# Performance work log

Measured on AMD Instinct MI355X. Metric: run time of the kernel, lower is better.

The kernel has to match this reference:

```python
import jax
import jax.numpy as jnp
import numpy as np

N_WIRES = 4          # hardcoded by QLayer encoder (rx on wires 0..3)
H = N_WIRES          # hidden_dim must equal n_qubits for the gating elementwise math
T, B, D, TAGS = 512, 2048, 8, 16  # original unbinds dim 0, so dim0 = time, dim1 = batch


def apply_rx(state, theta, wire):
    """Apply RX(theta) on `wire`. state: (B,2,2,2,2) complex64, theta: (B,)."""
    st = jnp.moveaxis(state, 1 + wire, -1)
    a, b = st[..., 0], st[..., 1]
    th = theta[:, None, None, None] * 0.5
    c = jnp.cos(th)
    s = -1j * jnp.sin(th)
    st = jnp.stack([c * a + s * b, s * a + c * b], axis=-1)
    return jnp.moveaxis(st, -1, 1 + wire)


def apply_cnot(state, ctrl, tgt):
    st = jnp.moveaxis(state, (1 + ctrl, 1 + tgt), (-2, -1))  # (...,2,2)
    st = st.at[..., 1, :].set(st[..., 1, ::-1])
    return jnp.moveaxis(st, (-2, -1), (1 + ctrl, 1 + tgt))


def qlayer(angles, thetas):
    """QuantumQLSTM.QLayer: RX data encoding, trainable RX, CNOT ring, PauliZ expvals.
    angles: (B, 4) data angles; thetas: (4,) trainable RX angles -> (B, 4) expvals."""
    bsz = angles.shape[0]
    state = jnp.zeros((bsz, 16), jnp.complex64).at[:, 0].set(1.0)
    state = state.reshape(bsz, 2, 2, 2, 2)
    for w in range(N_WIRES):
        state = apply_rx(state, angles[:, w], w)
    for w in range(N_WIRES):
        state = apply_rx(state, jnp.broadcast_to(thetas[w], (bsz,)), w)
    for w in range(N_WIRES):  # cnot(w, w+1), last wraps to 0
        state = apply_cnot(state, w, (w + 1) % N_WIRES)
    probs = state.real ** 2 + state.imag ** 2  # (B,2,2,2,2)
    exps = []
    for w in range(N_WIRES):
        sign = jnp.array([1.0, -1.0], jnp.float32).reshape(
            [1] + [2 if i == w else 1 for i in range(N_WIRES)])
        exps.append(jnp.sum(probs * sign, axis=(1, 2, 3, 4)))
    return jnp.stack(exps, axis=-1)  # (B, 4)


def lstm_forward(x, w_gates, b_gates, rx_theta):
    # Faithful to torch: inputs.unbind(dim=0) -> scan over axis 0; batch = x.shape[1].
    bsz = x.shape[1]
    h0 = jnp.zeros((bsz, H), x.dtype)
    c0 = jnp.zeros((bsz, H), x.dtype)

    def step(carry, xt):
        hx, cx = carry
        comb = jnp.concatenate([xt, hx], axis=-1)                    # (B, D+H)
        pre = jnp.einsum('bd,gkd->gbk', comb, w_gates) + b_gates[:, None, :]  # (4,B,4)
        f = jax.nn.sigmoid(qlayer(pre[0], rx_theta[0]))
        i = jax.nn.sigmoid(qlayer(pre[1], rx_theta[1]))
        g = jnp.tanh(qlayer(pre[2], rx_theta[2]))
        o = jax.nn.sigmoid(qlayer(pre[3], rx_theta[3]))
        cx = f * cx + i * g
        hx = o * jnp.tanh(cx)
        return (hx, cx), hx

    _, outs = jax.lax.scan(jax.checkpoint(step), (h0, c0), x)
    return outs  # (T, B, H)


def setup_inputs() -> dict:
    key = jax.random.key(0)
    ks = jax.random.split(key, 6)
    x = jax.random.normal(ks[0], (T, B, D), jnp.float32)
    w_gates = jax.random.normal(ks[1], (4, N_WIRES, D + H), jnp.float32) * 0.3
    b_gates = jnp.zeros((4, N_WIRES), jnp.float32)
    rx_theta = jax.random.uniform(ks[2], (4, N_WIRES), jnp.float32, 0.0, 2.0 * np.pi)
    w_tag = jax.random.normal(ks[3], (TAGS, H), jnp.float32) * 0.3
    b_tag = jnp.zeros((TAGS,), jnp.float32)
    return {"x": x, "w_gates": w_gates, "b_gates": b_gates,
            "rx_theta": rx_theta, "w_tag": w_tag, "b_tag": b_tag}


def reference(x, w_gates, b_gates, rx_theta, w_tag, b_tag):
    # encode(): SamplerQNN has input_params=[], so it cannot transform features;
    # features pass through to the QLSTM (see notes).
    outs = lstm_forward(x, w_gates, b_gates, rx_theta)   # (T, B, H)
    logits = outs @ w_tag.T + b_tag                      # (T, B, TAGS)
    return jax.nn.log_softmax(logits, axis=-1)
```

## Files before the change

kernel.cpp:

```cpp
#include <hip/hip_runtime.h>

#define TT   512
#define BB   2048
#define NTAG 16
#define CH   8
#define NCH  (TT / CH)
#define BBN  (BB * NTAG)

typedef float v2f __attribute__((ext_vector_type(2)));

#define DPP_XOR1  0xB1
#define DPP_XOR2  0x4E
#define DPP_XOR3  0x1B
#define DPP_ROR4  0x124
#define DPP_ROR8  0x128
#define DPP_ROR12 0x12C

template<int CTRL>
__device__ __forceinline__ float dppf(float v) {
    int r = __builtin_amdgcn_update_dpp(0, __builtin_bit_cast(int, v),
                                        CTRL, 0xF, 0xF, true);
    return __builtin_bit_cast(float, r);
}

#define PINV(x) asm volatile("" : "+v"(x))

__global__ __launch_bounds__(256, 1) void qlstm_fused(
    const float* __restrict__ x,
    const float* __restrict__ w_gates,
    const float* __restrict__ b_gates,
    const float* __restrict__ rx_theta,
    const float* __restrict__ w_tag,
    const float* __restrict__ b_tag,
    float* __restrict__ out)
{
    __shared__ float  accL[2][2][CH][64];
    __shared__ float  hrng[2][2][CH][64];
    __shared__ float4 xstg[2][2][64];

    const int tid = threadIdx.x;
    const int wv  = tid >> 6;
    const int l   = tid & 63;
    const int e   = l >> 4;
    const int g   = (l >> 2) & 3;
    const int k   = l & 3;

    const float IV  = 0.15915494309189535f;
    const float L2E = 1.44269504088896f;
    const float LN2 = 0.69314718056f;

    if (wv < 2) {
        const int s = wv;

        const float* wrow = w_gates + (g * 4 + k) * 12;
        float wh0 = wrow[8 + (k ^ 0)] * IV;
        float wh1 = wrow[8 + (k ^ 1)] * IV;
        float wh2 = wrow[8 + (k ^ 2)] * IV;
        float wh3 = wrow[8 + (k ^ 3)] * IV;

        const bool gt = (g == 2);
        float ab = gt ? 0.0f : 0.5f;
        float d0 = gt ? 0.999904f  : 0.25f;
        float d1 = gt ? -0.331065f : -0.0208333333f;
        float d2 = gt ? 0.120472f  : 0.00208333333f;
        float d3 = gt ? -0.027717f : -2.10813e-4f;

        float u0 = 0.999160f,  u1 = -0.325289f, u2 = 0.112257f;
        float u3 = -0.028766f, u4 = 0.0043665f, u5 = -0.00028186f;

        const bool k0 = (k == 0), k1 = (k == 1), k3 = (k == 3);
        const bool g0 = (g == 0), g2 = (g == 2), glo = (g < 2);

        PINV(wh0); PINV(wh1); PINV(wh2); PINV(wh3);
        PINV(ab);  PINV(d0);  PINV(d1);  PINV(d2);  PINV(d3);
        PINV(u0);  PINV(u1);  PINV(u2);  PINV(u3);  PINV(u4);  PINV(u5);

        float h = 0.f, h1 = 0.f, h2 = 0.f, h3 = 0.f, c = 0.f;

        __syncthreads();

        for (int cc = 0; cc < NCH; ++cc) {
            const int cur = cc & 1;

            const float* ap = &accL[s][cur][0][l];
            float a0 = ap[0 * 64], a1 = ap[1 * 64];
            float a2 = ap[2 * 64], a3 = ap[3 * 64];
            float a4 = ap[4 * 64], a5 = ap[5 * 64];
            float a6 = ap[6 * 64], a7 = ap[7 * 64];
            asm volatile("" : "+v"(a0), "+v"(a1), "+v"(a2), "+v"(a3),
                             "+v"(a4), "+v"(a5), "+v"(a6), "+v"(a7));
            float a[CH] = { a0, a1, a2, a3, a4, a5, a6, a7 };

            float* hp = &hrng[s][cur][0][l];

            #pragma unroll
            for (int i = 0; i < CH; ++i) {
                float ang = fmaf(h,  wh0, a[i]);
                ang = fmaf(h1, wh1, ang);
                ang = fmaf(h2, wh2, ang);
                ang = fmaf(h3, wh3, ang);

                const float C = __builtin_amdgcn_cosf(ang);
                const float m1 = dppf<DPP_XOR1>(C);
                const float m2 = dppf<DPP_XOR2>(C);
                const float m3 = dppf<DPP_XOR3>(C);
                const float Bp  = m2 * m3;
                const float pp  = C * m1;
                const float F1  = k0 ? m1 : C;
                const float F1b = k3 ? pp : F1;
                const float F2  = k1 ? m1 : Bp;
                const float q   = F1b * F2;

                const float y  = q * q;
                const float y2 = y * y;
                const float tA = fmaf(y, d1, d0);
                const float tB = fmaf(y, d3, d2);
                const float P  = fmaf(y2, tB, tA);
                const float act = fmaf(q, P, ab);

                const float rA = dppf<DPP_ROR12>(act);
                const float rB = dppf<DPP_ROR8>(act);
                const float rC = dppf<DPP_ROR4>(act);
                const float f_ = glo ? (g0 ? act : rC) : (g2 ? rB : rA);
                const float i_ = glo ? (g0 ? rA : act) : (g2 ? rC : rB);
                const float gg = glo ? (g0 ? rB : rA) : (g2 ? act : rC);
                const float o_ = glo ? (g0 ? rC : rB) : (g2 ? rA : act);

                c = fmaf(f_, c, i_ * gg);

                const float cy  = c * c;
                const float cy2 = cy * cy;
                const float t1  = fmaf(cy, u1, u0);
                const float t2  = fmaf(cy, u3, u2);
                const float t3  = fmaf(cy, u5, u4);
                const float t4  = fmaf(cy2, t3, t2);
                const float Pc  = fmaf(cy2, t4, t1);
                const float voc = o_ * c;
                const float hr  = Pc * voc;

                hp[i * 64] = hr;

                h  = hr;
                h1 = dppf<DPP_XOR1>(hr);
                h2 = dppf<DPP_XOR2>(hr);
                h3 = dppf<DPP_XOR3>(hr);
            }
            __syncthreads();
        }
    } else {
        const int s  = wv - 2;
        const int b0 = blockIdx.x * 8 + s * 4;

        const float* wrow = w_gates + (g * 4 + k) * 12;
        const v2f wp0 = { wrow[0] * IV, wrow[1] * IV };
        const v2f wp1 = { wrow[2] * IV, wrow[3] * IV };
        const v2f wp2 = { wrow[4] * IV, wrow[5] * IV };
        const v2f wp3 = { wrow[6] * IV, wrow[7] * IV };
        const v2f bp  = { (b_gates[g * 4 + k] + rx_theta[g * 4 + k]) * IV, 0.0f };

        const int tag = g * 4 + k;
        const float wt0 = w_tag[tag * 4 + (k ^ 0)] * L2E;
        const float wt1 = w_tag[tag * 4 + (k ^ 1)] * L2E;
        const float wt2 = w_tag[tag * 4 + (k ^ 2)] * L2E;
        const float wt3 = w_tag[tag * 4 + (k ^ 3)] * L2E;
        const float bt  = b_tag[tag] * L2E;

        const int hsl = e * 16 + k;
        float* outp = out + (size_t)b0 * NTAG + l;

        const float* xlane = x + (size_t)(l >> 3) * (BB * 8)
                               + (size_t)b0 * 8 + (l & 7) * 4;
        const size_t CHOFF = (size_t)CH * BB * 8;

        float4 reg = *(const float4*)(xlane);
        xstg[s][0][l] = reg;
        reg = *(const float4*)(xlane + CHOFF);
        xstg[s][1][l] = reg;
        {
            float* ap = &accL[s][0][0][l];
            #pragma unroll
            for (int i = 0; i < CH; ++i) {
                const float4 xA = xstg[s][0][i * 8 + 2 * e];
                const float4 xB = xstg[s][0][i * 8 + 2 * e + 1];
                const v2f a01 = { xA.x, xA.y }, a23 = { xA.z, xA.w };
                const v2f a45 = { xB.x, xB.y }, a67 = { xB.z, xB.w };
                v2f acc = __builtin_elementwise_fma(a01, wp0, bp);
                acc = __builtin_elementwise_fma(a23, wp1, acc);
                acc = __builtin_elementwise_fma(a45, wp2, acc);
                acc = __builtin_elementwise_fma(a67, wp3, acc);
                ap[i * 64] = acc.x + acc.y;
            }
        }
        reg = *(const float4*)(xlane + 2 * CHOFF);
        __syncthreads();

        for (int cc = 0; cc < NCH; ++cc) {
            const int cur = cc & 1;

            if (cc + 2 < NCH) {
                xstg[s][cur][l] = reg;
                const int cn = (cc + 3 < NCH) ? cc + 3 : NCH - 1;
                reg = *(const float4*)(xlane + (size_t)cn * CHOFF);
            }

            if (cc + 1 < NCH) {
                float* ap = &accL[s][cur ^ 1][0][l];
                #pragma unroll
                for (int i = 0; i < CH; ++i) {
                    const float4 xA = xstg[s][cur ^ 1][i * 8 + 2 * e];
                    const float4 xB = xstg[s][cur ^ 1][i * 8 + 2 * e + 1];
                    const v2f a01 = { xA.x, xA.y }, a23 = { xA.z, xA.w };
                    const v2f a45 = { xB.x, xB.y }, a67 = { xB.z, xB.w };
                    v2f acc = __builtin_elementwise_fma(a01, wp0, bp);
                    acc = __builtin_elementwise_fma(a23, wp1, acc);
                    acc = __builtin_elementwise_fma(a45, wp2, acc);
                    acc = __builtin_elementwise_fma(a67, wp3, acc);
                    ap[i * 64] = acc.x + acc.y;
                }
            }

            if (cc > 0) {
                const float* hp = &hrng[s][cur ^ 1][0][hsl];
                #pragma unroll
                for (int i = 0; i < CH; ++i) {
                    const float hv = hp[i * 64];
                    const float q1 = dppf<DPP_XOR1>(hv);
                    const float q2 = dppf<DPP_XOR2>(hv);
                    const float q3 = dppf<DPP_XOR3>(hv);

                    const float lgq = fmaf(hv, wt0, fmaf(q1, wt1, fmaf(q2, wt2,
                                         fmaf(q3, wt3, bt))));
                    const float ex = __builtin_amdgcn_exp2f(lgq);
                    float sm = ex + dppf<DPP_XOR1>(ex);
                    sm = sm + dppf<DPP_XOR2>(sm);
                    sm = sm + dppf<DPP_ROR4>(sm);
                    sm = sm + dppf<DPP_ROR8>(sm);
                    const float l2s = __builtin_amdgcn_logf(sm);

                    *outp = (lgq - l2s) * LN2;
                    outp += BBN;
                }
            }
            __syncthreads();
        }

        {
            const float* hp = &hrng[s][1][0][hsl];
            #pragma unroll
            for (int i = 0; i < CH; ++i) {
                const float hv = hp[i * 64];
                const float q1 = dppf<DPP_XOR1>(hv);
                const float q2 = dppf<DPP_XOR2>(hv);
                const float q3 = dppf<DPP_XOR3>(hv);

                const float lgq = fmaf(hv, wt0, fmaf(q1, wt1, fmaf(q2, wt2,
                                     fmaf(q3, wt3, bt))));
                const float ex = __builtin_amdgcn_exp2f(lgq);
                float sm = ex + dppf<DPP_XOR1>(ex);
                sm = sm + dppf<DPP_XOR2>(sm);
                sm = sm + dppf<DPP_ROR4>(sm);
                sm = sm + dppf<DPP_ROR8>(sm);
                const float l2s = __builtin_amdgcn_logf(sm);

                *outp = (lgq - l2s) * LN2;
                outp += BBN;
            }
        }
    }
}

extern "C" void kernel_launch(void* const* d_in, const int* in_sizes, int n_in,
                              void* d_out, int out_size, void* d_ws, size_t ws_size,
                              hipStream_t stream) {
    const float* x        = (const float*)d_in[0];
    const float* w_gates  = (const float*)d_in[1];
    const float* b_gates  = (const float*)d_in[2];
    const float* rx_theta = (const float*)d_in[3];
    const float* w_tag    = (const float*)d_in[4];
    const float* b_tag    = (const float*)d_in[5];
    float* out = (float*)d_out;

    qlstm_fused<<<BB / 8, 256, 0, stream>>>(x, w_gates, b_gates, rx_theta,
                                            w_tag, b_tag, out);
}
```

Measured before the change: 146.4 us.

## Transpose recurrent lane mapping so gate gather uses DPP quad broadcasts

Changes the lane layout of the recurrent waves so each quad holds the four gates of one wire instead of the four wires of one gate. The gate combination then uses quad-broadcast DPP moves with no select chains, and the wire mixing uses row rotations. The angle sum is split into two partial chains to shorten the serial dependency. The accumulator read index and the h-slot index of the producer waves are remapped to match, which risks mismatched indexing.

```diff
diff --git a/kernel.cpp b/kernel.cpp
--- a/kernel.cpp
+++ b/kernel.cpp
@@ -15,6 +15,10 @@
 #define DPP_ROR4  0x124
 #define DPP_ROR8  0x128
 #define DPP_ROR12 0x12C
+#define DPP_BC0   0x00
+#define DPP_BC1   0x55
+#define DPP_BC2   0xAA
+#define DPP_BC3   0xFF
 
 template<int CTRL>
 __device__ __forceinline__ float dppf(float v) {
@@ -42,8 +46,6 @@
     const int wv  = tid >> 6;
     const int l   = tid & 63;
     const int e   = l >> 4;
-    const int g   = (l >> 2) & 3;
-    const int k   = l & 3;
 
     const float IV  = 0.15915494309189535f;
     const float L2E = 1.44269504088896f;
@@ -51,14 +53,16 @@
 
     if (wv < 2) {
         const int s = wv;
-
-        const float* wrow = w_gates + (g * 4 + k) * 12;
-        float wh0 = wrow[8 + (k ^ 0)] * IV;
-        float wh1 = wrow[8 + (k ^ 1)] * IV;
-        float wh2 = wrow[8 + (k ^ 2)] * IV;
-        float wh3 = wrow[8 + (k ^ 3)] * IV;
-
-        const bool gt = (g == 2);
+        const int w = (l >> 2) & 3;
+        const int G = l & 3;
+
+        const float* wrow = w_gates + (G * 4 + w) * 12;
+        float wh0 = wrow[8 + ((w + 0) & 3)] * IV;
+        float wh1 = wrow[8 + ((w + 1) & 3)] * IV;
+        float wh2 = wrow[8 + ((w + 2) & 3)] * IV;
+        float wh3 = wrow[8 + ((w + 3) & 3)] * IV;
+
+        const bool gt = (G == 2);
         float ab = gt ? 0.0f : 0.5f;
         float d0 = gt ? 0.999904f  : 0.25f;
         float d1 = gt ? -0.331065f : -0.0208333333f;
@@ -68,21 +72,22 @@
         float u0 = 0.999160f,  u1 = -0.325289f, u2 = 0.112257f;
         float u3 = -0.028766f, u4 = 0.0043665f, u5 = -0.00028186f;
 
-        const bool k0 = (k == 0), k1 = (k == 1), k3 = (k == 3);
-        const bool g0 = (g == 0), g2 = (g == 2), glo = (g < 2);
+        const bool w0 = (w == 0), w1 = (w == 1), w3 = (w == 3);
 
         PINV(wh0); PINV(wh1); PINV(wh2); PINV(wh3);
         PINV(ab);  PINV(d0);  PINV(d1);  PINV(d2);  PINV(d3);
         PINV(u0);  PINV(u1);  PINV(u2);  PINV(u3);  PINV(u4);  PINV(u5);
 
-        float h = 0.f, h1 = 0.f, h2 = 0.f, h3 = 0.f, c = 0.f;
+        const int atl = (l & 48) | ((l & 3) << 2) | ((l >> 2) & 3);
+
+        float h = 0.f, hg1 = 0.f, hg2 = 0.f, hg3 = 0.f, c = 0.f;
 
         __syncthreads();
 
         for (int cc = 0; cc < NCH; ++cc) {
             const int cur = cc & 1;
 
-            const float* ap = &accL[s][cur][0][l];
+            const float* ap = &accL[s][cur][0][atl];
             float a0 = ap[0 * 64], a1 = ap[1 * 64];
             float a2 = ap[2 * 64], a3 = ap[3 * 64];
             float a4 = ap[4 * 64], a5 = ap[5 * 64];
@@ -95,20 +100,22 @@
 
             #pragma unroll
             for (int i = 0; i < CH; ++i) {
-                float ang = fmaf(h,  wh0, a[i]);
-                ang = fmaf(h1, wh1, ang);
-                ang = fmaf(h2, wh2, ang);
-                ang = fmaf(h3, wh3, ang);
+                const float sA  = fmaf(h, wh0, a[i]);
+                const float td1 = fmaf(hg1, wh1, sA);
+                const float td2 = hg2 * wh2;
+                const float td3 = fmaf(hg3, wh3, td2);
+                const float ang = td1 + td3;
 
                 const float C = __builtin_amdgcn_cosf(ang);
-                const float m1 = dppf<DPP_XOR1>(C);
-                const float m2 = dppf<DPP_XOR2>(C);
-                const float m3 = dppf<DPP_XOR3>(C);
-                const float Bp  = m2 * m3;
-                const float pp  = C * m1;
-                const float F1  = k0 ? m1 : C;
-                const float F1b = k3 ? pp : F1;
-                const float F2  = k1 ? m1 : Bp;
+
+                const float n1 = dppf<DPP_ROR12>(C);
+                const float n2 = dppf<DPP_ROR8>(C);
+                const float n3 = dppf<DPP_ROR4>(C);
+                const float Bp = n2 * n3;
+                const float pp = C * n1;
+                const float F1  = w0 ? n1 : C;
+                const float F1b = w3 ? pp : F1;
+                const float F2  = w1 ? n3 : Bp;
                 const float q   = F1b * F2;
 
                 const float y  = q * q;
@@ -118,15 +125,12 @@
                 const float P  = fmaf(y2, tB, tA);
                 const float act = fmaf(q, P, ab);
 
-                const float rA = dppf<DPP_ROR12>(act);
-                const float rB = dppf<DPP_ROR8>(act);
-                const float rC = dppf<DPP_ROR4>(act);
-                const float f_ = glo ? (g0 ? act : rC) : (g2 ? rB : rA);
-                const float i_ = glo ? (g0 ? rA : act) : (g2 ? rC : rB);
-                const float gg = glo ? (g0 ? rB : rA) : (g2 ? act : rC);
-                const float o_ = glo ? (g0 ? rC : rB) : (g2 ? rA : act);
-
-                c = fmaf(f_, c, i_ * gg);
+                const float F_ = dppf<DPP_BC0>(act);
+                const float A1 = dppf<DPP_BC1>(act);
+                const float A2 = dppf<DPP_BC2>(act);
+                const float O_ = dppf<DPP_BC3>(act);
+
+                c = fmaf(F_, c, A1 * A2);
 
                 const float cy  = c * c;
                 const float cy2 = cy * cy;
@@ -135,21 +139,23 @@
                 const float t3  = fmaf(cy, u5, u4);
                 const float t4  = fmaf(cy2, t3, t2);
                 const float Pc  = fmaf(cy2, t4, t1);
-                const float voc = o_ * c;
+                const float voc = O_ * c;
                 const float hr  = Pc * voc;
 
                 hp[i * 64] = hr;
 
-                h  = hr;
-                h1 = dppf<DPP_XOR1>(hr);
-                h2 = dppf<DPP_XOR2>(hr);
-                h3 = dppf<DPP_XOR3>(hr);
+                h   = hr;
+                hg1 = dppf<DPP_ROR12>(hr);
+                hg2 = dppf<DPP_ROR8>(hr);
+                hg3 = dppf<DPP_ROR4>(hr);
             }
             __syncthreads();
         }
     } else {
         const int s  = wv - 2;
         const int b0 = blockIdx.x * 8 + s * 4;
+        const int g  = (l >> 2) & 3;
+        const int k  = l & 3;
 
         const float* wrow = w_gates + (g * 4 + k) * 12;
         const v2f wp0 = { wrow[0] * IV, wrow[1] * IV };
@@ -165,7 +171,7 @@
         const float wt3 = w_tag[tag * 4 + (k ^ 3)] * L2E;
         const float bt  = b_tag[tag] * L2E;
 
-        const int hsl = e * 16 + k;
+        const int hsl = e * 16 + k * 4;
         float* outp = out + (size_t)b0 * NTAG + l;
 
         const float* xlane = x + (size_t)(l >> 3) * (BB * 8)
```

Result: faster. 137.6 us (-6.0%).
